# Performance work log

Measured on AMD Instinct MI355X. Metric: run time of the kernel, lower is better.

The kernel has to match this reference:

```python
import jax, jax.numpy as jnp
import numpy as np

D_MODEL = 1024
NUM_HEADS = 16
HEAD_DIM = D_MODEL // NUM_HEADS


def setup_inputs() -> dict:
    key = jax.random.key(0)
    ks = jax.random.split(key, 5)
    x = jax.random.normal(ks[0], (4, 2048, D_MODEL), dtype=jnp.float32)
    # xavier_uniform with gain=0.1 for square (D,D) weights: limit = 0.1*sqrt(6/(D+D))
    limit = 0.1 * np.sqrt(6.0 / (2 * D_MODEL))
    def w(k):
        return jax.random.uniform(k, (D_MODEL, D_MODEL), jnp.float32, -limit, limit)
    return {
        "x": x,
        "W_q": w(ks[1]), "b_q": jnp.zeros((D_MODEL,), jnp.float32),
        "W_k": w(ks[2]), "b_k": jnp.zeros((D_MODEL,), jnp.float32),
        "W_v": w(ks[3]), "b_v": jnp.zeros((D_MODEL,), jnp.float32),
        "W_o": w(ks[4]), "b_o": jnp.zeros((D_MODEL,), jnp.float32),
    }


def reference(x, W_q, b_q, W_k, b_k, W_v, b_v, W_o, b_o):
    B, S, D = x.shape
    H, Hd = NUM_HEADS, HEAD_DIM
    # Linear: x @ W^T + b (torch nn.Linear convention); weights here are (out, in)
    def proj(W, b):
        y = jnp.einsum('bsd,ed->bse', x, W) + b
        return y.reshape(B, S, H, Hd).transpose(0, 2, 1, 3)  # [B,H,S,Hd]
    Q = proj(W_q, b_q)
    K = proj(W_k, b_k)
    V = proj(W_v, b_v)
    scale = 1.0 / np.sqrt(Hd).astype(np.float32)
    scores = jnp.einsum('bhqd,bhkd->bhqk', Q, K) * scale  # [B,H,S,S]
    attn = jax.nn.softmax(scores, axis=-1)
    ctx = jnp.einsum('bhqk,bhkd->bhqd', attn, V)
    ctx = ctx.transpose(0, 2, 1, 3).reshape(B, S, D)
    out = jnp.einsum('bsd,ed->bse', ctx, W_o) + b_o
    return out
```

## Files before the change

kernel.cpp:

```cpp
#include <hip/hip_runtime.h>
#include <math.h>

#define B_  4
#define S_  2048
#define D_  1024
#define H_  16
#define HD_ 64
#define M_  (B_*S_)

typedef short short8 __attribute__((ext_vector_type(8)));
typedef float f32x4 __attribute__((ext_vector_type(4)));

#define MFMA16(a,b,c) __builtin_amdgcn_mfma_f32_16x16x32_bf16(a, b, c, 0, 0, 0)

#if __has_builtin(__builtin_amdgcn_exp2f)
#define EXP2(x) __builtin_amdgcn_exp2f(x)
#else
#define EXP2(x) exp2f(x)
#endif

__device__ __forceinline__ unsigned short f2bf(float f) {
    unsigned u = __float_as_uint(f);
    u = (u + 0x7FFF + ((u >> 16) & 1)) >> 16;
    return (unsigned short)u;
}

__device__ __forceinline__ unsigned pack_bf16(float a, float b) {
#if __has_builtin(__builtin_amdgcn_cvt_pk_bf16_f32)
    typedef __bf16 bf2 __attribute__((ext_vector_type(2)));
    bf2 v = __builtin_amdgcn_cvt_pk_bf16_f32(a, b);
    unsigned r;
    __builtin_memcpy(&r, &v, 4);
    return r;
#else
    unsigned ua = __float_as_uint(a), ub = __float_as_uint(b);
    ua += 0x7FFFu + ((ua >> 16) & 1u);
    ub += 0x7FFFu + ((ub >> 16) & 1u);
    return __builtin_amdgcn_perm(ub, ua, 0x07060302u);
#endif
}

__device__ __forceinline__ void async_copy16(const void* g, void* l) {
    __builtin_amdgcn_global_load_lds(
        (const __attribute__((address_space(1))) void*)g,
        (__attribute__((address_space(3))) void*)l, 16, 0, 0);
}

__global__ __launch_bounds__(256) void cvt_all(
    const float* __restrict__ x,
    const float* __restrict__ w0, const float* __restrict__ w1,
    const float* __restrict__ w2, const float* __restrict__ w3,
    unsigned short* __restrict__ xb, unsigned short* __restrict__ wb)
{
    size_t i = ((size_t)blockIdx.x * 256 + threadIdx.x) * 4;
    const float* src; unsigned short* dst;
    if (i < (size_t)M_ * D_) {
        src = x + i; dst = xb + i;
    } else {
        size_t j = i - (size_t)M_ * D_;
        int z = (int)(j >> 20);
        const float* w = (z == 0) ? w0 : (z == 1) ? w1 : (z == 2) ? w2 : w3;
        src = w + (j & ((size_t)D_ * D_ - 1)); dst = wb + j;
    }
    float4 v = *(const float4*)src;
    uint2 o;
    o.x = pack_bf16(v.x, v.y);
    o.y = pack_bf16(v.z, v.w);
    *(uint2*)dst = o;
}

__global__ __launch_bounds__(512, 2) void qkv8(
    const unsigned short* __restrict__ A,
    const unsigned short* __restrict__ W,
    const float* __restrict__ bq, const float* __restrict__ bk,
    const float* __restrict__ bv,
    unsigned short* __restrict__ Qo, unsigned short* __restrict__ Ko,
    unsigned short* __restrict__ Vo)
{
    __shared__ unsigned short As[2][256 * 64];
    __shared__ unsigned short Ws[2][256 * 64];
    const int K = D_;
    int tid = threadIdx.x;
    int w = tid >> 6, lane = tid & 63;
    int quad = lane >> 4, l16 = lane & 15;
    int r8 = lane >> 3, c8 = lane & 7;
    int cK = c8 ^ r8;
    int wm = w >> 2, wn = w & 3;
    int m0 = blockIdx.y * 256, n0 = blockIdx.x * 256;
    int fl = l16 & 7;

    int z = n0 >> 10;
    const float* bias = (z == 0) ? bq : (z == 1) ? bk : bv;
    unsigned short* out = (z == 0) ? Qo : (z == 1) ? Ko : Vo;
    float cscale = (z == 0) ? 0.125f * 1.44269504088896f : 1.0f;

    f32x4 acc[8][4];
    #pragma unroll
    for (int i = 0; i < 8; ++i)
        #pragma unroll
        for (int j = 0; j < 4; ++j)
            acc[i][j] = (f32x4){0.f, 0.f, 0.f, 0.f};

    const unsigned short* Ag = A + (size_t)(m0 + w * 8 + r8) * K + cK * 8;
    const unsigned short* Wg = W + (size_t)(n0 + w * 8 + r8) * K + cK * 8;

    auto stageA = [&](int slot, int kt) {
        #pragma unroll
        for (int ii = 0; ii < 4; ++ii)
            async_copy16(Ag + (size_t)(ii * 64) * K + kt * 64,
                         &As[slot][(ii * 64 + w * 8) * 64]);
    };
    auto stageW = [&](int slot, int kt) {
        #pragma unroll
        for (int ii = 0; ii < 4; ++ii)
            async_copy16(Wg + (size_t)(ii * 64) * K + kt * 64,
                         &Ws[slot][(ii * 64 + w * 8) * 64]);
    };

    stageA(0, 0);
    stageW(0, 0);
    __syncthreads();

    #define RDA(cur, i, s) (*(const short8*)&As[cur][(wm * 128 + (i) * 16 + l16) * 64 + \
                             (((quad + (s) * 4) ^ fl) * 8)])
    #define RDB(cur, j, s) (*(const short8*)&Ws[cur][(wn * 64 + (j) * 16 + l16) * 64 + \
                             (((quad + (s) * 4) ^ fl) * 8)])

    for (int kt = 0; kt < 16; ++kt) {
        int cur = kt & 1;
        bool pre = (kt < 15);
        short8 a[4][2], b0[2][2], b1[2][2];

        #pragma unroll
        for (int i = 0; i < 4; ++i)
            #pragma unroll
            for (int s = 0; s < 2; ++s) a[i][s] = RDA(cur, i, s);
        #pragma unroll
        for (int j = 0; j < 2; ++j)
            #pragma unroll
            for (int s = 0; s < 2; ++s) b0[j][s] = RDB(cur, j, s);
        if (pre) stageA(cur ^ 1, kt + 1);
        __builtin_amdgcn_s_setprio(1);
        #pragma unroll
        for (int i = 0; i < 4; ++i)
            #pragma unroll
            for (int j = 0; j < 2; ++j)
                #pragma unroll
                for (int s = 0; s < 2; ++s)
                    acc[i][j] = MFMA16(a[i][s], b0[j][s], acc[i][j]);
        __builtin_amdgcn_s_setprio(0);
        __builtin_amdgcn_s_barrier();
        __builtin_amdgcn_sched_barrier(0);

        #pragma unroll
        for (int j = 0; j < 2; ++j)
            #pragma unroll
            for (int s = 0; s < 2; ++s) b1[j][s] = RDB(cur, j + 2, s);
        if (pre) stageW(cur ^ 1, kt + 1);
        __builtin_amdgcn_s_setprio(1);
        #pragma unroll
        for (int i = 0; i < 4; ++i)
            #pragma unroll
            for (int j = 0; j < 2; ++j)
                #pragma unroll
                for (int s = 0; s < 2; ++s)
                    acc[i][j + 2] = MFMA16(a[i][s], b1[j][s], acc[i][j + 2]);
        __builtin_amdgcn_s_setprio(0);
        __builtin_amdgcn_s_barrier();
        __builtin_amdgcn_sched_barrier(0);

        #pragma unroll
        for (int i = 0; i < 4; ++i)
            #pragma unroll
            for (int s = 0; s < 2; ++s) a[i][s] = RDA(cur, i + 4, s);
        __builtin_amdgcn_s_setprio(1);
        #pragma unroll
        for (int i = 0; i < 4; ++i)
            #pragma unroll
            for (int j = 0; j < 2; ++j)
                #pragma unroll
                for (int s = 0; s < 2; ++s)
                    acc[i + 4][j + 2] = MFMA16(a[i][s], b1[j][s], acc[i + 4][j + 2]);
        __builtin_amdgcn_s_setprio(0);
        __builtin_amdgcn_s_barrier();
        __builtin_amdgcn_sched_barrier(0);

        __builtin_amdgcn_s_setprio(1);
        #pragma unroll
        for (int i = 0; i < 4; ++i)
            #pragma unroll
            for (int j = 0; j < 2; ++j)
                #pragma unroll
                for (int s = 0; s < 2; ++s)
                    acc[i + 4][j] = MFMA16(a[i][s], b0[j][s], acc[i + 4][j]);
        __builtin_amdgcn_s_setprio(0);
        asm volatile("s_waitcnt vmcnt(0)" ::: "memory");
        __builtin_amdgcn_s_barrier();
        __builtin_amdgcn_sched_barrier(0);
    }
    #undef RDA
    #undef RDB

    #pragma unroll
    for (int i = 0; i < 8; ++i) {
        int mb = m0 + wm * 128 + i * 16 + quad * 4;
        #pragma unroll
        for (int j = 0; j < 4; ++j) {
            int n = n0 + wn * 64 + j * 16 + l16;
            int nn = n & 1023;
            float bn = bias[nn];
            int h = nn >> 6, hd = nn & 63;
            if (z != 2) {
                #pragma unroll
                for (int r = 0; r < 4; ++r) {
                    int m = mb + r;
                    int bb = m >> 11, s = m & (S_ - 1);
                    out[(((size_t)(bb * H_ + h)) * S_ + s) * HD_ + hd] =
                        f2bf((acc[i][j][r] + bn) * cscale);
                }
            } else {
                int bb = mb >> 11, s0 = mb & (S_ - 1);
                uint2 o;
                o.x = pack_bf16(acc[i][j][0] + bn, acc[i][j][1] + bn);
                o.y = pack_bf16(acc[i][j][2] + bn, acc[i][j][3] + bn);
                *(uint2*)&out[(((size_t)(bb * H_ + h)) * HD_ + hd) * S_ + s0] = o;
            }
        }
    }
}

__device__ __forceinline__ void gemm_body(
    const unsigned short* __restrict__ A, const unsigned short* __restrict__ W,
    const float* __restrict__ bias, void* __restrict__ out,
    int mode, float cscale, int bx, int by)
{
    __shared__ unsigned short As[128 * 64];
    __shared__ unsigned short Ws[128 * 64];
    const int K = D_;
    int tid = threadIdx.x;
    int w = tid >> 6, lane = tid & 63;
    int quad = lane >> 4, l16 = lane & 15;
    int r8 = lane >> 3, c8 = lane & 7;
    int cK = c8 ^ r8;
    int wm = w >> 2, wn = w & 3;
    int m0 = by * 128, n0 = bx * 128;
    int fl = l16 & 7;

    f32x4 acc[4][2];
    #pragma unroll
    for (int i = 0; i < 4; ++i)
        #pragma unroll
        for (int j = 0; j < 2; ++j)
            acc[i][j] = (f32x4){0.f, 0.f, 0.f, 0.f};

    const unsigned short* Ag = A + (size_t)(m0 + w * 8 + r8) * K + cK * 8;
    const unsigned short* Wg = W + (size_t)(n0 + w * 8 + r8) * K + cK * 8;

    for (int k0 = 0; k0 < K; k0 += 64) {
        __syncthreads();
        #pragma unroll
        for (int ii = 0; ii < 2; ++ii) {
            async_copy16(Ag + k0 + (size_t)ii * 64 * K, As + (ii * 64 + w * 8) * 64);
            async_copy16(Wg + k0 + (size_t)ii * 64 * K, Ws + (ii * 64 + w * 8) * 64);
        }
        __syncthreads();
        #pragma unroll
        for (int s = 0; s < 2; ++s) {
            int st = ((quad + s * 4) ^ fl) * 8;
            short8 a[4], b[2];
            #pragma unroll
            for (int i = 0; i < 4; ++i)
                a[i] = *(const short8*)&As[(wm * 64 + i * 16 + l16) * 64 + st];
            #pragma unroll
            for (int j = 0; j < 2; ++j)
                b[j] = *(const short8*)&Ws[(wn * 32 + j * 16 + l16) * 64 + st];
            #pragma unroll
            for (int i = 0; i < 4; ++i)
                #pragma unroll
                for (int j = 0; j < 2; ++j)
                    acc[i][j] = MFMA16(a[i], b[j], acc[i][j]);
        }
    }

    #pragma unroll
    for (int i = 0; i < 4; ++i) {
        int mb = m0 + wm * 64 + i * 16 + quad * 4;
        #pragma unroll
        for (int j = 0; j < 2; ++j) {
            int n = n0 + wn * 32 + j * 16 + l16;
            float bn = bias[n];
            if (mode == 0) {
                #pragma unroll
                for (int r = 0; r < 4; ++r)
                    ((float*)out)[(size_t)(mb + r) * D_ + n] = acc[i][j][r] + bn;
            } else if (mode == 1) {
                int h = n >> 6, hd = n & 63;
                #pragma unroll
                for (int r = 0; r < 4; ++r) {
                    int m = mb + r;
                    int bb = m >> 11, s = m & (S_ - 1);
                    ((unsigned short*)out)[(((size_t)(bb * H_ + h)) * S_ + s) * HD_ + hd] =
                        f2bf((acc[i][j][r] + bn) * cscale);
                }
            } else {
                int h = n >> 6, hd = n & 63;
                int bb = mb >> 11, s0 = mb & (S_ - 1);
                uint2 o;
                o.x = pack_bf16(acc[i][j][0] + bn, acc[i][j][1] + bn);
                o.y = pack_bf16(acc[i][j][2] + bn, acc[i][j][3] + bn);
                *(uint2*)&((unsigned short*)out)[(((size_t)(bb * H_ + h)) * HD_ + hd) * S_ + s0] = o;
            }
        }
    }
}

__global__ __launch_bounds__(512) void out_gemm(
    const unsigned short* __restrict__ A, const unsigned short* __restrict__ W,
    const float* __restrict__ bias, float* __restrict__ out)
{
    gemm_body(A, W, bias, out, 0, 1.0f, blockIdx.x, blockIdx.y);
}

__global__ __launch_bounds__(512, 4) void attn_mfma(
    const unsigned short* __restrict__ Q, const unsigned short* __restrict__ K,
    const unsigned short* __restrict__ VT, unsigned short* __restrict__ ctx)
{
    __shared__ unsigned short Ks[2 * 64 * 64];
    __shared__ unsigned short VTs[2 * 64 * 64];
    __shared__ unsigned short QPs[256 * 64];

    int tid = threadIdx.x;
    int w = tid >> 6, lane = tid & 63;
    int quad = lane >> 4, l16 = lane & 15;
    int r8 = lane >> 3, c8 = lane & 7;
    int cK = c8 ^ r8;
    int fl  = l16 & 7;
    int fl2 = (l16 ^ (l16 >> 1)) & 7;
    int bh = blockIdx.x;
    int q0 = blockIdx.y * 256;

    const unsigned short* Qp = Q + ((size_t)bh * S_ + q0) * HD_;
    const unsigned short* Kp = K + (size_t)bh * S_ * HD_;
    const unsigned short* Vp = VT + (size_t)bh * HD_ * S_;

    int cQ = c8 ^ r8 ^ (r8 >> 1) ^ ((w & 1) * 4);
    #pragma unroll
    for (int ii = 0; ii < 4; ++ii)
        async_copy16(Qp + (size_t)(ii * 64 + w * 8 + r8) * HD_ + cQ * 8,
                     QPs + (ii * 64 + w * 8) * 64);
    async_copy16(Kp + (size_t)(w * 8 + r8) * HD_ + cK * 8, Ks + (w * 8) * 64);
    async_copy16(Vp + (size_t)(w * 8 + r8) * S_ + cK * 8, VTs + (w * 8) * 64);
    __syncthreads();

    short8 bq_[2][2];
    #pragma unroll
    for (int mt = 0; mt < 2; ++mt)
        #pragma unroll
        for (int s = 0; s < 2; ++s)
            bq_[mt][s] = *(const short8*)&QPs[(w * 32 + mt * 16 + l16) * 64 +
                                              (((quad + s * 4) ^ fl2) * 8)];

    f32x4 O[2][4];
    float lsum[2] = {0.f, 0.f};
    #pragma unroll
    for (int mt = 0; mt < 2; ++mt)
        #pragma unroll
        for (int nt = 0; nt < 4; ++nt) O[mt][nt] = (f32x4){0.f, 0.f, 0.f, 0.f};

    int cur = 0;
    for (int kt = 0; kt < S_ / 64; ++kt) {
        if (kt + 1 < S_ / 64) {
            int nb = (cur ^ 1) * 4096;
            async_copy16(Kp + (size_t)((kt + 1) * 64 + w * 8 + r8) * HD_ + cK * 8,
                         Ks + nb + (w * 8) * 64);
            async_copy16(Vp + (size_t)(w * 8 + r8) * S_ + (kt + 1) * 64 + cK * 8,
                         VTs + nb + (w * 8) * 64);
        }
        const unsigned short* ks  = Ks + cur * 4096;
        const unsigned short* vts = VTs + cur * 4096;

        f32x4 sc[2][4];
        #pragma unroll
        for (int mt = 0; mt < 2; ++mt)
            #pragma unroll
            for (int nt = 0; nt < 4; ++nt) sc[mt][nt] = (f32x4){0.f, 0.f, 0.f, 0.f};
        __builtin_amdgcn_s_setprio(1);
        #pragma unroll
        for (int s = 0; s < 2; ++s) {
            int stk = ((quad + s * 4) ^ fl) * 8;
            #pragma unroll
            for (int nt = 0; nt < 4; ++nt) {
                short8 ak = *(const short8*)&ks[(nt * 16 + l16) * 64 + stk];
                sc[0][nt] = MFMA16(ak, bq_[0][s], sc[0][nt]);
                sc[1][nt] = MFMA16(ak, bq_[1][s], sc[1][nt]);
            }
        }
        __builtin_amdgcn_s_setprio(0);

        #pragma unroll
        for (int mt = 0; mt < 2; ++mt) {
            #pragma unroll
            for (int nt = 0; nt < 4; ++nt) {
                float p0 = EXP2(sc[mt][nt][0]);
                float p1 = EXP2(sc[mt][nt][1]);
                float p2 = EXP2(sc[mt][nt][2]);
                float p3 = EXP2(sc[mt][nt][3]);
                lsum[mt] += (p0 + p1) + (p2 + p3);
                uint2 pk;
                pk.x = pack_bf16(p0, p1);
                pk.y = pack_bf16(p2, p3);
                int addr = (w * 32 + mt * 16 + l16) * 64 +
                           (((nt * 2 + (quad >> 1)) ^ fl2) * 8) + (quad & 1) * 4;
                *(uint2*)&QPs[addr] = pk;
            }
        }

        __builtin_amdgcn_s_setprio(1);
        #pragma unroll
        for (int s = 0; s < 2; ++s) {
            int stp = ((quad + s * 4) ^ fl2) * 8;
            int stv = ((quad + s * 4) ^ fl) * 8;
            short8 pa0 = *(const short8*)&QPs[(w * 32 + l16) * 64 + stp];
            short8 pa1 = *(const short8*)&QPs[(w * 32 + 16 + l16) * 64 + stp];
            #pragma unroll
            for (int nt = 0; nt < 4; ++nt) {
                short8 bv_ = *(const short8*)&vts[(nt * 16 + l16) * 64 + stv];
                O[0][nt] = MFMA16(pa0, bv_, O[0][nt]);
                O[1][nt] = MFMA16(pa1, bv_, O[1][nt]);
            }
        }
        __builtin_amdgcn_s_setprio(0);

        __syncthreads();
        cur ^= 1;
    }

    float linv[2];
    #pragma unroll
    for (int mt = 0; mt < 2; ++mt) {
        float l = lsum[mt];
        l += __shfl_xor(l, 16);
        l += __shfl_xor(l, 32);
        linv[mt] = 1.0f / l;
    }

    int b = bh >> 4, h = bh & (H_ - 1);
    #pragma unroll
    for (int mt = 0; mt < 2; ++mt)
        #pragma unroll
        for (int r = 0; r < 4; ++r) {
            float inv = __shfl(linv[mt], quad * 4 + r, 64);
            int q = q0 + w * 32 + mt * 16 + quad * 4 + r;
            size_t base = ((size_t)(b * S_) + q) * D_ + h * HD_;
            #pragma unroll
            for (int nt = 0; nt < 4; ++nt)
                ctx[base + nt * 16 + l16] = f2bf(O[mt][nt][r] * inv);
        }
}

extern "C" void kernel_launch(void* const* d_in, const int* in_sizes, int n_in,
                              void* d_out, int out_size, void* d_ws, size_t ws_size,
                              hipStream_t stream) {
    const float* x  = (const float*)d_in[0];
    const float* Wq = (const float*)d_in[1];
    const float* bq = (const float*)d_in[2];
    const float* Wk = (const float*)d_in[3];
    const float* bk = (const float*)d_in[4];
    const float* Wv = (const float*)d_in[5];
    const float* bv = (const float*)d_in[6];
    const float* Wo = (const float*)d_in[7];
    const float* bo = (const float*)d_in[8];

    unsigned short* xb  = (unsigned short*)d_ws;
    unsigned short* wb  = xb + (size_t)M_ * D_;
    unsigned short* Qb  = wb + (size_t)4 * D_ * D_;
    unsigned short* Kb  = Qb + (size_t)M_ * D_;
    unsigned short* VTb = Kb + (size_t)M_ * D_;
    unsigned short* ctb = VTb + (size_t)M_ * D_;

    int cvt_blocks = (M_ * D_ + 4 * D_ * D_) / 1024;
    cvt_all<<<cvt_blocks, 256, 0, stream>>>(x, Wq, Wk, Wv, Wo, xb, wb);

    qkv8<<<dim3(3 * D_ / 256, M_ / 256), 512, 0, stream>>>(
        xb, wb, bq, bk, bv, Qb, Kb, VTb);

    attn_mfma<<<dim3(B_ * H_, S_ / 256), 512, 0, stream>>>(Qb, Kb, VTb, ctb);

    out_gemm<<<dim3(D_ / 128, M_ / 128), 512, 0, stream>>>(
        ctb, wb + (size_t)3 * D_ * D_, bo, (float*)d_out);
}
```

Measured before the change: 280.3 us.

## Triple-buffer attention K/V loads and swizzle GEMM block order

The attention kernel moves from double to triple buffering of K and V^T tiles. It prefetches two tiles ahead and replaces the full __syncthreads with a partial vmcnt wait plus a raw barrier, so global-load latency overlaps more of the compute. The setprio hints are removed. The QKV and output GEMMs remap block indices with a grouped swizzle to improve L2 reuse of weight and activation tiles. Triple buffering raises LDS use per block, which may reduce occupancy, and the hand-counted vmcnt wait relies on the exact number of outstanding loads being right.

```diff
diff --git a/kernel.cpp b/kernel.cpp
--- a/kernel.cpp
+++ b/kernel.cpp
@@ -86,7 +86,11 @@
     int r8 = lane >> 3, c8 = lane & 7;
     int cK = c8 ^ r8;
     int wm = w >> 2, wn = w & 3;
-    int m0 = blockIdx.y * 256, n0 = blockIdx.x * 256;
+
+    int lin = blockIdx.x + 12 * blockIdx.y;
+    int swz = (lin & 7) * 48 + (lin >> 3);
+    int by = swz / 12, bx = swz % 12;
+    int m0 = by * 256, n0 = bx * 256;
     int fl = l16 & 7;
 
     int z = n0 >> 10;
@@ -318,15 +322,17 @@
     const unsigned short* __restrict__ A, const unsigned short* __restrict__ W,
     const float* __restrict__ bias, float* __restrict__ out)
 {
-    gemm_body(A, W, bias, out, 0, 1.0f, blockIdx.x, blockIdx.y);
+    int lin = blockIdx.x + 8 * blockIdx.y;
+    int swz = (lin & 7) * 64 + (lin >> 3);
+    gemm_body(A, W, bias, out, 0, 1.0f, swz & 7, swz >> 3);
 }
 
 __global__ __launch_bounds__(512, 4) void attn_mfma(
     const unsigned short* __restrict__ Q, const unsigned short* __restrict__ K,
     const unsigned short* __restrict__ VT, unsigned short* __restrict__ ctx)
 {
-    __shared__ unsigned short Ks[2 * 64 * 64];
-    __shared__ unsigned short VTs[2 * 64 * 64];
+    __shared__ unsigned short Ks[3 * 64 * 64];
+    __shared__ unsigned short VTs[3 * 64 * 64];
     __shared__ unsigned short QPs[256 * 64];
 
     int tid = threadIdx.x;
@@ -348,8 +354,13 @@
     for (int ii = 0; ii < 4; ++ii)
         async_copy16(Qp + (size_t)(ii * 64 + w * 8 + r8) * HD_ + cQ * 8,
                      QPs + (ii * 64 + w * 8) * 64);
-    async_copy16(Kp + (size_t)(w * 8 + r8) * HD_ + cK * 8, Ks + (w * 8) * 64);
-    async_copy16(Vp + (size_t)(w * 8 + r8) * S_ + cK * 8, VTs + (w * 8) * 64);
+    #pragma unroll
+    for (int t = 0; t < 2; ++t) {
+        async_copy16(Kp + (size_t)(t * 64 + w * 8 + r8) * HD_ + cK * 8,
+                     Ks + t * 4096 + (w * 8) * 64);
+        async_copy16(Vp + (size_t)(w * 8 + r8) * S_ + t * 64 + cK * 8,
+                     VTs + t * 4096 + (w * 8) * 64);
+    }
     __syncthreads();
 
     short8 bq_[2][2];
@@ -367,24 +378,23 @@
         #pragma unroll
         for (int nt = 0; nt < 4; ++nt) O[mt][nt] = (f32x4){0.f, 0.f, 0.f, 0.f};
 
-    int cur = 0;
-    for (int kt = 0; kt < S_ / 64; ++kt) {
-        if (kt + 1 < S_ / 64) {
-            int nb = (cur ^ 1) * 4096;
-            async_copy16(Kp + (size_t)((kt + 1) * 64 + w * 8 + r8) * HD_ + cK * 8,
+    const int NT = S_ / 64;
+    for (int kt = 0; kt < NT; ++kt) {
+        if (kt + 2 < NT) {
+            int nb = ((kt + 2) % 3) * 4096;
+            async_copy16(Kp + (size_t)((kt + 2) * 64 + w * 8 + r8) * HD_ + cK * 8,
                          Ks + nb + (w * 8) * 64);
-            async_copy16(Vp + (size_t)(w * 8 + r8) * S_ + (kt + 1) * 64 + cK * 8,
+            async_copy16(Vp + (size_t)(w * 8 + r8) * S_ + (kt + 2) * 64 + cK * 8,
                          VTs + nb + (w * 8) * 64);
         }
-        const unsigned short* ks  = Ks + cur * 4096;
-        const unsigned short* vts = VTs + cur * 4096;
+        const unsigned short* ks  = Ks + (kt % 3) * 4096;
+        const unsigned short* vts = VTs + (kt % 3) * 4096;
 
         f32x4 sc[2][4];
         #pragma unroll
         for (int mt = 0; mt < 2; ++mt)
             #pragma unroll
             for (int nt = 0; nt < 4; ++nt) sc[mt][nt] = (f32x4){0.f, 0.f, 0.f, 0.f};
-        __builtin_amdgcn_s_setprio(1);
         #pragma unroll
         for (int s = 0; s < 2; ++s) {
             int stk = ((quad + s * 4) ^ fl) * 8;
@@ -395,7 +405,6 @@
                 sc[1][nt] = MFMA16(ak, bq_[1][s], sc[1][nt]);
             }
         }
-        __builtin_amdgcn_s_setprio(0);
 
         #pragma unroll
         for (int mt = 0; mt < 2; ++mt) {
@@ -415,7 +424,6 @@
             }
         }
 
-        __builtin_amdgcn_s_setprio(1);
         #pragma unroll
         for (int s = 0; s < 2; ++s) {
             int stp = ((quad + s * 4) ^ fl2) * 8;
@@ -429,10 +437,11 @@
                 O[1][nt] = MFMA16(pa1, bv_, O[1][nt]);
             }
         }
-        __builtin_amdgcn_s_setprio(0);
-
-        __syncthreads();
-        cur ^= 1;
+
+        if (kt + 2 < NT) asm volatile("s_waitcnt vmcnt(2)" ::: "memory");
+        else             asm volatile("s_waitcnt vmcnt(0)" ::: "memory");
+        __builtin_amdgcn_s_barrier();
+        __builtin_amdgcn_sched_barrier(0);
     }
 
     float linv[2];
```

Measured after the change: 268.0 us. 1.05x faster.
